# Optimization experiments

Hardware: AMD Instinct MI355X
Metric: run time of the kernel (lower is better)

Reference implementation:

```python
import jax, jax.numpy as jnp
import numpy as np

N_NODES = 100000
N_EDGES = 1600000
N_GRAPHS = 64
D_IN = 3
HIDDEN = 256
N_CLASSES = 10
NEG_SLOPE = 0.01  # torch F.leaky_relu default


def gcn_conv(x, W, b, src, dst, n_nodes):
    """GCNConv: D^{-1/2}(A+I)D^{-1/2} X W + b with self-loops."""
    h = x @ W  # [N, H]
    ones = jnp.ones(src.shape[0], h.dtype)
    deg = jax.ops.segment_sum(ones, dst, num_segments=n_nodes) + 1.0  # +1 self-loop
    dinv = jax.lax.rsqrt(deg)
    coef = dinv[src] * dinv[dst]  # [E]
    agg = jax.ops.segment_sum(h[src] * coef[:, None], dst, num_segments=n_nodes)
    agg = agg + h * (1.0 / deg)[:, None]  # self-loop contribution (norm = 1/deg)
    return agg + b


def leaky_relu(v):
    return jnp.where(v >= 0, v, NEG_SLOPE * v)


def setup_inputs() -> dict:
    key = jax.random.key(0)
    ks = jax.random.split(key, 12)
    x = jax.random.normal(ks[0], (N_NODES, D_IN), dtype=jnp.float32)
    edge_index = jax.random.randint(ks[1], (2, N_EDGES), 0, N_NODES, dtype=jnp.int32)
    batch = jnp.sort(jax.random.randint(ks[2], (N_NODES,), 0, N_GRAPHS, dtype=jnp.int32))
    s1 = 1.0 / np.sqrt(D_IN)
    s2 = 1.0 / np.sqrt(HIDDEN)
    W1 = jax.random.uniform(ks[3], (D_IN, HIDDEN), jnp.float32, -s1, s1)
    b1 = jnp.zeros((HIDDEN,), jnp.float32)
    W2 = jax.random.uniform(ks[4], (HIDDEN, HIDDEN), jnp.float32, -s2, s2)
    b2 = jnp.zeros((HIDDEN,), jnp.float32)
    W3 = jax.random.uniform(ks[5], (HIDDEN, HIDDEN), jnp.float32, -s2, s2)
    b3 = jnp.zeros((HIDDEN,), jnp.float32)
    Wc = jax.random.uniform(ks[6], (HIDDEN, N_CLASSES), jnp.float32, -s2, s2)
    bc = jax.random.uniform(ks[7], (N_CLASSES,), jnp.float32, -s2, s2)
    return {"x": x, "edge_index": edge_index, "batch": batch,
            "W1": W1, "b1": b1, "W2": W2, "b2": b2, "W3": W3, "b3": b3,
            "Wc": Wc, "bc": bc}


def reference(x, edge_index, batch, W1, b1, W2, b2, W3, b3, Wc, bc):
    src, dst = edge_index[0], edge_index[1]
    h = leaky_relu(gcn_conv(x, W1, b1, src, dst, N_NODES))
    h = leaky_relu(gcn_conv(h, W2, b2, src, dst, N_NODES))
    h = leaky_relu(gcn_conv(h, W3, b3, src, dst, N_NODES))
    # global mean pool over graphs
    sums = jax.ops.segment_sum(h, batch, num_segments=N_GRAPHS)
    cnt = jax.ops.segment_sum(jnp.ones((N_NODES,), h.dtype), batch, num_segments=N_GRAPHS)
    pooled = sums / jnp.maximum(cnt, 1.0)[:, None]  # [G, H]
    logits = pooled @ Wc + bc
    return jax.nn.softmax(logits, axis=1)
```

## Files before the change

### kernel.cpp

```cpp
#include <hip/hip_runtime.h>
#include <hip/hip_bf16.h>
#include <cstdint>
#include <cstddef>

#define N_NODES   100000
#define N_EDGES   1600000
#define N_GRAPHS  64
#define HIDDEN    256
#define N_CLASSES 10
#define NEG_SLOPE 0.01f

#define E_PAD    (N_EDGES + 8 * N_NODES)
#define N_RANGES 8
#define R_SIZE   ((N_NODES + N_RANGES - 1) / N_RANGES)
#define CHUNK    2048
#define GEMM_BLOCKS 391

typedef __attribute__((ext_vector_type(4))) float f32x4;
typedef __attribute__((ext_vector_type(2))) float f32x2;

__device__ __forceinline__ float bf2f(unsigned short u) {
    return __uint_as_float(((unsigned int)u) << 16);
}

__device__ __forceinline__ unsigned char f2fp8(float v) {
    return (unsigned char)(__builtin_amdgcn_cvt_pk_fp8_f32(v, v, 0, false) & 0xff);
}

__global__ void k_deg_hist(const int* __restrict__ dst, int* __restrict__ cnt) {
    int e = (blockIdx.x * 256 + threadIdx.x) * 4;
    if (e >= N_EDGES) return;
    int4 d4 = *(const int4*)(dst + e);
    atomicAdd(&cnt[d4.x], 1);
    atomicAdd(&cnt[d4.y], 1);
    atomicAdd(&cnt[d4.z], 1);
    atomicAdd(&cnt[d4.w], 1);
}

__global__ void k_graph_bounds(const int* __restrict__ batch,
                               int* __restrict__ gstart, int* __restrict__ gcnt) {
    int g = threadIdx.x;
    int lo = 0, hi = N_NODES;
    while (lo < hi) { int mid = (lo + hi) >> 1; if (batch[mid] < g) lo = mid + 1; else hi = mid; }
    __shared__ int sh[N_GRAPHS + 1];
    sh[g] = lo;
    if (g == 0) sh[N_GRAPHS] = N_NODES;
    __syncthreads();
    gstart[g] = sh[g];
    gcnt[g]   = sh[g + 1] - sh[g];
}

__global__ void k_dinv(const int* __restrict__ cnt, float* __restrict__ dinv) {
    int i = blockIdx.x * 256 + threadIdx.x;
    if (i < N_NODES) dinv[i] = rsqrtf((float)cnt[i] + 1.0f);
}

__global__ void k_scanA(const int* __restrict__ cnt, int* __restrict__ out, int* __restrict__ bsum) {
    __shared__ int sh[256];
    int tid = threadIdx.x;
    int base = blockIdx.x * 1024 + tid * 4;
    int v[4]; int s = 0;
#pragma unroll
    for (int i = 0; i < 4; i++) {
        int idx = base + i;
        v[i] = (idx < N_NODES) ? ((cnt[idx] + 7) & ~7) : 0;
        s += v[i];
    }
    sh[tid] = s; __syncthreads();
    for (int off = 1; off < 256; off <<= 1) {
        int t = (tid >= off) ? sh[tid - off] : 0;
        __syncthreads();
        sh[tid] += t;
        __syncthreads();
    }
    int excl = sh[tid] - s;
    if (tid == 255) bsum[blockIdx.x] = sh[255];
#pragma unroll
    for (int i = 0; i < 4; i++) { int idx = base + i; if (idx < N_NODES) out[idx] = excl; excl += v[i]; }
}

__global__ void k_scanB(int* __restrict__ bsum, int nb) {
    __shared__ int sh[128];
    int tid = threadIdx.x;
    int v = (tid < nb) ? bsum[tid] : 0;
    sh[tid] = v; __syncthreads();
    for (int off = 1; off < 128; off <<= 1) {
        int t = (tid >= off) ? sh[tid - off] : 0;
        __syncthreads();
        sh[tid] += t;
        __syncthreads();
    }
    if (tid < nb) bsum[tid] = sh[tid] - v;
}

__global__ void k_scanC(int* __restrict__ off_arr, const int* __restrict__ bsum,
                        int* __restrict__ cursor, const int* __restrict__ cnt,
                        int2* __restrict__ rec) {
    int i = blockIdx.x * 256 + threadIdx.x;
    if (i < N_NODES) {
        int v = off_arr[i] + bsum[i >> 10];
        off_arr[i] = v;
        cursor[i]  = v;
        int c  = cnt[i];
        int cp = (c + 7) & ~7;
        for (int p = v + c; p < v + cp; ++p) rec[p] = make_int2(0, 0);
        if (i == N_NODES - 1) off_arr[N_NODES] = v + cp;
    }
}

__global__ __launch_bounds__(256) void k_fill(const int* __restrict__ src, const int* __restrict__ dst,
                                              const float* __restrict__ dinv,
                                              int* __restrict__ cursor, int2* __restrict__ rec) {
    int b = blockIdx.x;
    int r = b & (N_RANGES - 1);
    int lo = r * R_SIZE, hi = lo + R_SIZE;
    int e0 = (b >> 3) * CHUNK + threadIdx.x * 8;
    if (e0 >= N_EDGES) return;
    if (e0 + 8 <= N_EDGES) {
        int4 da = *(const int4*)(dst + e0);
        int4 db = *(const int4*)(dst + e0 + 4);
        int d[8] = {da.x, da.y, da.z, da.w, db.x, db.y, db.z, db.w};
#pragma unroll
        for (int j = 0; j < 8; ++j) {
            if (d[j] >= lo && d[j] < hi) {
                int s = src[e0 + j];
                float c = dinv[s] * dinv[d[j]];
                int p = atomicAdd(&cursor[d[j]], 1);
                rec[p] = make_int2(s, __float_as_int(c));
            }
        }
    } else {
        for (int j = 0; j < 8 && e0 + j < N_EDGES; ++j) {
            int dj = dst[e0 + j];
            if (dj >= lo && dj < hi) {
                int s = src[e0 + j];
                float c = dinv[s] * dinv[dj];
                int p = atomicAdd(&cursor[dj], 1);
                rec[p] = make_int2(s, __float_as_int(c));
            }
        }
    }
}

__global__ void k_wprep(const float* __restrict__ W, unsigned char* __restrict__ Wswz) {
    int n = blockIdx.x; int k = threadIdx.x;
    unsigned char v = f2fp8(W[k * HIDDEN + n]);
    int k0 = k >> 5, nt = n >> 4;
    int lane = (((k >> 3) & 3) << 4) | (n & 15);
    int j = k & 7;
    Wswz[(size_t)(((k0 * 16) + nt) * 64 + lane) * 8 + j] = v;
}

__global__ void k_agg3(const float* __restrict__ x, const int* __restrict__ off,
                       const int2* __restrict__ rec, const float* __restrict__ dinv,
                       float4* __restrict__ ax) {
    int i = blockIdx.x * 256 + threadIdx.x;
    if (i >= N_NODES) return;
    float di = dinv[i];
    float selfc = di * di;
    float a0 = x[i * 3 + 0] * selfc, a1 = x[i * 3 + 1] * selfc, a2 = x[i * 3 + 2] * selfc;
    int e = off[i], e1 = off[i + 1];
    for (; e < e1; e += 4) {
        const int4* rp = (const int4*)(rec + e);
        int4 r01 = rp[0];
        int4 r23 = rp[1];
        int s0 = r01.x, s1 = r01.z, s2 = r23.x, s3 = r23.z;
        float c0 = __int_as_float(r01.y), c1 = __int_as_float(r01.w);
        float c2 = __int_as_float(r23.y), c3 = __int_as_float(r23.w);
        a0 += c0 * x[s0 * 3 + 0] + c1 * x[s1 * 3 + 0] + c2 * x[s2 * 3 + 0] + c3 * x[s3 * 3 + 0];
        a1 += c0 * x[s0 * 3 + 1] + c1 * x[s1 * 3 + 1] + c2 * x[s2 * 3 + 1] + c3 * x[s3 * 3 + 1];
        a2 += c0 * x[s0 * 3 + 2] + c1 * x[s1 * 3 + 2] + c2 * x[s2 * 3 + 2] + c3 * x[s3 * 3 + 2];
    }
    ax[i] = make_float4(a0, a1, a2, 0.f);
}

__global__ void k_l1(const float4* __restrict__ ax, const float* __restrict__ W1,
                     const float* __restrict__ b1, unsigned char* __restrict__ out) {
    int node = blockIdx.x; int c = threadIdx.x;
    float4 a = ax[node];
    float v = a.x * W1[c] + a.y * W1[HIDDEN + c] + a.z * W1[2 * HIDDEN + c] + b1[c];
    v = v >= 0.f ? v : NEG_SLOPE * v;
    out[(size_t)node * HIDDEN + c] = f2fp8(v);
}

__global__ __launch_bounds__(512, 2) void k_gemm_mfma(const unsigned char* __restrict__ A,
                                                      const unsigned char* __restrict__ Wswz,
                                                      unsigned char* __restrict__ C, int M) {
    __shared__ long Bs[8192];
    int tid = threadIdx.x;
    {
        const float4* gsrc = (const float4*)Wswz;
        float4* ldst = (float4*)Bs;
#pragma unroll
        for (int i = 0; i < 8; ++i) ldst[tid + 512 * i] = gsrc[tid + 512 * i];
    }
    __syncthreads();
    int lane = tid & 63, wv = tid >> 6;
    int quad = lane >> 4, r = lane & 15;
    int nstrips = M >> 4;
    for (int s = blockIdx.x * 8 + wv; s < nstrips; s += gridDim.x * 8) {
        int m0 = s * 16;
        const long* Ab = (const long*)(A + (size_t)(m0 + r) * HIDDEN) + quad;
        long af[8];
#pragma unroll
        for (int k0 = 0; k0 < 8; ++k0) af[k0] = Ab[k0 * 4];
#pragma unroll
        for (int half = 0; half < 2; ++half) {
            f32x4 acc[8];
#pragma unroll
            for (int i = 0; i < 8; i++) acc[i] = (f32x4){0.f, 0.f, 0.f, 0.f};
#pragma unroll
            for (int k0 = 0; k0 < 8; ++k0) {
#pragma unroll
                for (int nt = 0; nt < 8; ++nt) {
                    long b = Bs[(k0 * 16 + half * 8 + nt) * 64 + lane];
                    acc[nt] = __builtin_amdgcn_mfma_f32_16x16x32_fp8_fp8(af[k0], b, acc[nt], 0, 0, 0);
                }
            }
#pragma unroll
            for (int nt = 0; nt < 8; ++nt) {
#pragma unroll
                for (int i = 0; i < 4; ++i) {
                    int row = m0 + quad * 4 + i;
                    C[(size_t)row * HIDDEN + (half * 8 + nt) * 16 + r] = f2fp8(acc[nt][i]);
                }
            }
        }
    }
}

__global__ __launch_bounds__(256) void k_agg(const unsigned char* __restrict__ h,
                                             const float* __restrict__ bias,
                                             const int* __restrict__ off, const int2* __restrict__ rec,
                                             const float* __restrict__ dinv,
                                             unsigned char* __restrict__ out) {
    int node = (blockIdx.x * 256 + threadIdx.x) >> 6;
    int lane = threadIdx.x & 63;
    if (node >= N_NODES) return;
    float di = dinv[node];
    float selfc = di * di;
    unsigned int hv = *(const unsigned int*)(h + (size_t)node * HIDDEN + lane * 4);
    f32x2 hlo = __builtin_amdgcn_cvt_pk_f32_fp8(hv, false);
    f32x2 hhi = __builtin_amdgcn_cvt_pk_f32_fp8(hv, true);
    float4 bv = ((const float4*)bias)[lane];
    float4 acc = make_float4(bv.x + hlo.x * selfc, bv.y + hlo.y * selfc,
                             bv.z + hhi.x * selfc, bv.w + hhi.y * selfc);
    int e = off[node], e1 = off[node + 1];
    for (; e < e1; e += 8) {
        const int4* rp = (const int4*)(rec + e);
        int4 ra = rp[0];
        int4 rb = rp[1];
        int4 rc = rp[2];
        int4 rd = rp[3];
        unsigned int w0 = *(const unsigned int*)(h + (size_t)ra.x * HIDDEN + lane * 4);
        unsigned int w1 = *(const unsigned int*)(h + (size_t)ra.z * HIDDEN + lane * 4);
        unsigned int w2 = *(const unsigned int*)(h + (size_t)rb.x * HIDDEN + lane * 4);
        unsigned int w3 = *(const unsigned int*)(h + (size_t)rb.z * HIDDEN + lane * 4);
        unsigned int w4 = *(const unsigned int*)(h + (size_t)rc.x * HIDDEN + lane * 4);
        unsigned int w5 = *(const unsigned int*)(h + (size_t)rc.z * HIDDEN + lane * 4);
        unsigned int w6 = *(const unsigned int*)(h + (size_t)rd.x * HIDDEN + lane * 4);
        unsigned int w7 = *(const unsigned int*)(h + (size_t)rd.z * HIDDEN + lane * 4);
        float c0 = __int_as_float(ra.y), c1 = __int_as_float(ra.w);
        float c2 = __int_as_float(rb.y), c3 = __int_as_float(rb.w);
        float c4 = __int_as_float(rc.y), c5 = __int_as_float(rc.w);
        float c6 = __int_as_float(rd.y), c7 = __int_as_float(rd.w);
        f32x2 l0 = __builtin_amdgcn_cvt_pk_f32_fp8(w0, false), g0 = __builtin_amdgcn_cvt_pk_f32_fp8(w0, true);
        f32x2 l1 = __builtin_amdgcn_cvt_pk_f32_fp8(w1, false), g1 = __builtin_amdgcn_cvt_pk_f32_fp8(w1, true);
        f32x2 l2 = __builtin_amdgcn_cvt_pk_f32_fp8(w2, false), g2 = __builtin_amdgcn_cvt_pk_f32_fp8(w2, true);
        f32x2 l3 = __builtin_amdgcn_cvt_pk_f32_fp8(w3, false), g3 = __builtin_amdgcn_cvt_pk_f32_fp8(w3, true);
        f32x2 l4 = __builtin_amdgcn_cvt_pk_f32_fp8(w4, false), g4 = __builtin_amdgcn_cvt_pk_f32_fp8(w4, true);
        f32x2 l5 = __builtin_amdgcn_cvt_pk_f32_fp8(w5, false), g5 = __builtin_amdgcn_cvt_pk_f32_fp8(w5, true);
        f32x2 l6 = __builtin_amdgcn_cvt_pk_f32_fp8(w6, false), g6 = __builtin_amdgcn_cvt_pk_f32_fp8(w6, true);
        f32x2 l7 = __builtin_amdgcn_cvt_pk_f32_fp8(w7, false), g7 = __builtin_amdgcn_cvt_pk_f32_fp8(w7, true);
        acc.x += c0 * l0.x + c1 * l1.x + c2 * l2.x + c3 * l3.x
               + c4 * l4.x + c5 * l5.x + c6 * l6.x + c7 * l7.x;
        acc.y += c0 * l0.y + c1 * l1.y + c2 * l2.y + c3 * l3.y
               + c4 * l4.y + c5 * l5.y + c6 * l6.y + c7 * l7.y;
        acc.z += c0 * g0.x + c1 * g1.x + c2 * g2.x + c3 * g3.x
               + c4 * g4.x + c5 * g5.x + c6 * g6.x + c7 * g7.x;
        acc.w += c0 * g0.y + c1 * g1.y + c2 * g2.y + c3 * g3.y
               + c4 * g4.y + c5 * g5.y + c6 * g6.y + c7 * g7.y;
    }
    acc.x = acc.x >= 0.f ? acc.x : NEG_SLOPE * acc.x;
    acc.y = acc.y >= 0.f ? acc.y : NEG_SLOPE * acc.y;
    acc.z = acc.z >= 0.f ? acc.z : NEG_SLOPE * acc.z;
    acc.w = acc.w >= 0.f ? acc.w : NEG_SLOPE * acc.w;
    unsigned int pk = __builtin_amdgcn_cvt_pk_fp8_f32(acc.x, acc.y, 0, false);
    pk = __builtin_amdgcn_cvt_pk_fp8_f32(acc.z, acc.w, pk, true);
    *(unsigned int*)(out + (size_t)node * HIDDEN + lane * 4) = pk;
}

__global__ void k_pool(const unsigned char* __restrict__ h, const int* __restrict__ gstart,
                       const int* __restrict__ gcnt, float* __restrict__ pooled) {
    int g = blockIdx.x, chunk = blockIdx.y, t = threadIdx.x;
    int s = gstart[g], c = gcnt[g];
    int i0 = s + (int)(((long long)c * chunk) / 16);
    int i1 = s + (int)(((long long)c * (chunk + 1)) / 16);
    float acc = 0.f;
    for (int i = i0; i < i1; ++i) {
        f32x2 v = __builtin_amdgcn_cvt_pk_f32_fp8((unsigned int)h[(size_t)i * HIDDEN + t], false);
        acc += v.x;
    }
    atomicAdd(&pooled[g * HIDDEN + t], acc);
}

__global__ void k_head(const float* __restrict__ pooled, const int* __restrict__ gcnt,
                       const float* __restrict__ Wc, const float* __restrict__ bc,
                       float* __restrict__ out) {
    int g = blockIdx.x; int l = threadIdx.x;
    float inv = 1.0f / fmaxf((float)gcnt[g], 1.0f);
    float p[4];
#pragma unroll
    for (int i = 0; i < 4; i++) p[i] = pooled[g * HIDDEN + l + i * 64] * inv;
    __shared__ float logits[N_CLASSES];
#pragma unroll
    for (int j = 0; j < N_CLASSES; j++) {
        float s = 0.f;
#pragma unroll
        for (int i = 0; i < 4; i++) s += p[i] * Wc[(l + i * 64) * N_CLASSES + j];
        for (int o = 32; o > 0; o >>= 1) s += __shfl_down(s, o, 64);
        if (l == 0) logits[j] = s + bc[j];
    }
    __syncthreads();
    if (l == 0) {
        float m = logits[0];
        for (int j = 1; j < N_CLASSES; j++) m = fmaxf(m, logits[j]);
        float e[N_CLASSES]; float sum = 0.f;
        for (int j = 0; j < N_CLASSES; j++) { e[j] = expf(logits[j] - m); sum += e[j]; }
        for (int j = 0; j < N_CLASSES; j++) out[g * N_CLASSES + j] = e[j] / sum;
    }
}

extern "C" void kernel_launch(void* const* d_in, const int* in_sizes, int n_in,
                              void* d_out, int out_size, void* d_ws, size_t ws_size,
                              hipStream_t stream) {
    const float* x     = (const float*)d_in[0];
    const int*   edge  = (const int*)d_in[1];
    const int*   batch = (const int*)d_in[2];
    const float* W1 = (const float*)d_in[3];
    const float* b1 = (const float*)d_in[4];
    const float* W2 = (const float*)d_in[5];
    const float* b2 = (const float*)d_in[6];
    const float* W3 = (const float*)d_in[7];
    const float* b3 = (const float*)d_in[8];
    const float* Wc = (const float*)d_in[9];
    const float* bc = (const float*)d_in[10];
    float* out = (float*)d_out;
    const int* srcp = edge;
    const int* dstp = edge + N_EDGES;

    char* ws = (char*)d_ws;
    size_t off = 0;
    auto alloc = [&](size_t bytes) -> char* {
        char* p = ws + off;
        off += (bytes + 255) & ~(size_t)255;
        return p;
    };
    unsigned char* hA   = (unsigned char*)alloc((size_t)N_NODES * HIDDEN);
    unsigned char* hB   = (unsigned char*)alloc((size_t)N_NODES * HIDDEN);
    unsigned char* Wz2  = (unsigned char*)alloc((size_t)HIDDEN * HIDDEN);
    unsigned char* Wz3  = (unsigned char*)alloc((size_t)HIDDEN * HIDDEN);
    int*   deg_cnt  = (int*)alloc((size_t)N_NODES * 4);
    float* dinv     = (float*)alloc((size_t)N_NODES * 4);
    int*   csr_off  = (int*)alloc((size_t)(N_NODES + 1) * 4);
    int*   cursor   = (int*)alloc((size_t)N_NODES * 4);
    int2*  csr_rec  = (int2*)alloc((size_t)E_PAD * 8);
    float4* ax      = (float4*)alloc((size_t)N_NODES * 16);
    int*   gcnt     = (int*)alloc((size_t)N_GRAPHS * 4);
    int*   gstart   = (int*)alloc((size_t)N_GRAPHS * 4);
    float* pooled   = (float*)alloc((size_t)N_GRAPHS * HIDDEN * 4);
    int*   bsum     = (int*)alloc(128 * 4);

    hipMemsetAsync(deg_cnt, 0, (size_t)N_NODES * 4, stream);
    hipMemsetAsync(pooled, 0, (size_t)N_GRAPHS * HIDDEN * 4, stream);

    int eb4 = (N_EDGES / 4 + 255) / 256;
    int nb  = (N_NODES + 255) / 256;
    int sblocks = (N_NODES + 1023) / 1024;
    int fillb = N_RANGES * ((N_EDGES + CHUNK - 1) / CHUNK);

    k_deg_hist<<<eb4, 256, 0, stream>>>(dstp, deg_cnt);
    k_graph_bounds<<<1, 64, 0, stream>>>(batch, gstart, gcnt);
    k_dinv<<<nb, 256, 0, stream>>>(deg_cnt, dinv);
    k_scanA<<<sblocks, 256, 0, stream>>>(deg_cnt, csr_off, bsum);
    k_scanB<<<1, 128, 0, stream>>>(bsum, sblocks);
    k_scanC<<<nb, 256, 0, stream>>>(csr_off, bsum, cursor, deg_cnt, csr_rec);
    k_fill<<<fillb, 256, 0, stream>>>(srcp, dstp, dinv, cursor, csr_rec);
    k_wprep<<<HIDDEN, HIDDEN, 0, stream>>>(W2, Wz2);
    k_wprep<<<HIDDEN, HIDDEN, 0, stream>>>(W3, Wz3);

    k_agg3<<<nb, 256, 0, stream>>>(x, csr_off, csr_rec, dinv, ax);
    k_l1<<<N_NODES, 256, 0, stream>>>(ax, W1, b1, hA);

    int aggb = (N_NODES + 3) / 4;
    k_gemm_mfma<<<GEMM_BLOCKS, 512, 0, stream>>>(hA, Wz2, hB, N_NODES);
    k_agg<<<aggb, 256, 0, stream>>>(hB, b2, csr_off, csr_rec, dinv, hA);
    k_gemm_mfma<<<GEMM_BLOCKS, 512, 0, stream>>>(hA, Wz3, hB, N_NODES);
    k_agg<<<aggb, 256, 0, stream>>>(hB, b3, csr_off, csr_rec, dinv, hA);
    dim3 pg(N_GRAPHS, 16);
    k_pool<<<pg, 256, 0, stream>>>(hA, gstart, gcnt, pooled);
    k_head<<<N_GRAPHS, 64, 0, stream>>>(pooled, gcnt, Wc, bc, out);
}
```

Baseline: 550.4 us.

## Range-partition degree histogram, add nontemporal edge loads, pad x to float4

The degree histogram now uses the same dst-range partitioned blocks as the fill kernel, so each block's atomics land in one eighth of the node array. Edge and CSR record reads in fill and both aggregation kernels become nontemporal vector loads, keeping streamed data from pushing gathered features out of cache. The input features are padded to float4 by a new kernel so layer-1 aggregation gathers one vector per neighbour instead of three scalars. The tail-guard branch in fill is removed, which relies on N_EDGES being a multiple of 8. The histogram now reads dst eight times, and the extra launch and buffer add cost.

```diff
diff --git a/kernel.cpp b/kernel.cpp
--- a/kernel.cpp
+++ b/kernel.cpp
@@ -18,6 +18,7 @@
 
 typedef __attribute__((ext_vector_type(4))) float f32x4;
 typedef __attribute__((ext_vector_type(2))) float f32x2;
+typedef __attribute__((ext_vector_type(4))) int   v4i;
 
 __device__ __forceinline__ float bf2f(unsigned short u) {
     return __uint_as_float(((unsigned int)u) << 16);
@@ -27,14 +28,19 @@
     return (unsigned char)(__builtin_amdgcn_cvt_pk_fp8_f32(v, v, 0, false) & 0xff);
 }
 
-__global__ void k_deg_hist(const int* __restrict__ dst, int* __restrict__ cnt) {
-    int e = (blockIdx.x * 256 + threadIdx.x) * 4;
-    if (e >= N_EDGES) return;
-    int4 d4 = *(const int4*)(dst + e);
-    atomicAdd(&cnt[d4.x], 1);
-    atomicAdd(&cnt[d4.y], 1);
-    atomicAdd(&cnt[d4.z], 1);
-    atomicAdd(&cnt[d4.w], 1);
+__global__ __launch_bounds__(256) void k_deg_hist(const int* __restrict__ dst, int* __restrict__ cnt) {
+    int b = blockIdx.x;
+    int r = b & (N_RANGES - 1);
+    int lo = r * R_SIZE, hi = lo + R_SIZE;
+    int e0 = (b >> 3) * CHUNK + threadIdx.x * 8;
+    if (e0 >= N_EDGES) return;
+    v4i da = __builtin_nontemporal_load((const v4i*)(dst + e0));
+    v4i db = __builtin_nontemporal_load((const v4i*)(dst + e0 + 4));
+    int d[8] = {da.x, da.y, da.z, da.w, db.x, db.y, db.z, db.w};
+#pragma unroll
+    for (int j = 0; j < 8; ++j) {
+        if (d[j] >= lo && d[j] < hi) atomicAdd(&cnt[d[j]], 1);
+    }
 }
 
 __global__ void k_graph_bounds(const int* __restrict__ batch,
@@ -53,6 +59,11 @@
 __global__ void k_dinv(const int* __restrict__ cnt, float* __restrict__ dinv) {
     int i = blockIdx.x * 256 + threadIdx.x;
     if (i < N_NODES) dinv[i] = rsqrtf((float)cnt[i] + 1.0f);
+}
+
+__global__ void k_xpad(const float* __restrict__ x, float4* __restrict__ xp) {
+    int i = blockIdx.x * 256 + threadIdx.x;
+    if (i < N_NODES) xp[i] = make_float4(x[i * 3 + 0], x[i * 3 + 1], x[i * 3 + 2], 0.f);
 }
 
 __global__ void k_scanA(const int* __restrict__ cnt, int* __restrict__ out, int* __restrict__ bsum) {
@@ -116,28 +127,18 @@
     int lo = r * R_SIZE, hi = lo + R_SIZE;
     int e0 = (b >> 3) * CHUNK + threadIdx.x * 8;
     if (e0 >= N_EDGES) return;
-    if (e0 + 8 <= N_EDGES) {
-        int4 da = *(const int4*)(dst + e0);
-        int4 db = *(const int4*)(dst + e0 + 4);
-        int d[8] = {da.x, da.y, da.z, da.w, db.x, db.y, db.z, db.w};
-#pragma unroll
-        for (int j = 0; j < 8; ++j) {
-            if (d[j] >= lo && d[j] < hi) {
-                int s = src[e0 + j];
-                float c = dinv[s] * dinv[d[j]];
-                int p = atomicAdd(&cursor[d[j]], 1);
-                rec[p] = make_int2(s, __float_as_int(c));
-            }
-        }
-    } else {
-        for (int j = 0; j < 8 && e0 + j < N_EDGES; ++j) {
-            int dj = dst[e0 + j];
-            if (dj >= lo && dj < hi) {
-                int s = src[e0 + j];
-                float c = dinv[s] * dinv[dj];
-                int p = atomicAdd(&cursor[dj], 1);
-                rec[p] = make_int2(s, __float_as_int(c));
-            }
+    v4i da = __builtin_nontemporal_load((const v4i*)(dst + e0));
+    v4i db = __builtin_nontemporal_load((const v4i*)(dst + e0 + 4));
+    v4i sa = __builtin_nontemporal_load((const v4i*)(src + e0));
+    v4i sb = __builtin_nontemporal_load((const v4i*)(src + e0 + 4));
+    int d[8] = {da.x, da.y, da.z, da.w, db.x, db.y, db.z, db.w};
+    int s[8] = {sa.x, sa.y, sa.z, sa.w, sb.x, sb.y, sb.z, sb.w};
+#pragma unroll
+    for (int j = 0; j < 8; ++j) {
+        if (d[j] >= lo && d[j] < hi) {
+            float c = dinv[s[j]] * dinv[d[j]];
+            int p = atomicAdd(&cursor[d[j]], 1);
+            rec[p] = make_int2(s[j], __float_as_int(c));
         }
     }
 }
@@ -151,25 +152,26 @@
     Wswz[(size_t)(((k0 * 16) + nt) * 64 + lane) * 8 + j] = v;
 }
 
-__global__ void k_agg3(const float* __restrict__ x, const int* __restrict__ off,
+__global__ void k_agg3(const float4* __restrict__ xp, const int* __restrict__ off,
                        const int2* __restrict__ rec, const float* __restrict__ dinv,
                        float4* __restrict__ ax) {
     int i = blockIdx.x * 256 + threadIdx.x;
     if (i >= N_NODES) return;
     float di = dinv[i];
     float selfc = di * di;
-    float a0 = x[i * 3 + 0] * selfc, a1 = x[i * 3 + 1] * selfc, a2 = x[i * 3 + 2] * selfc;
+    float4 xi = xp[i];
+    float a0 = xi.x * selfc, a1 = xi.y * selfc, a2 = xi.z * selfc;
     int e = off[i], e1 = off[i + 1];
     for (; e < e1; e += 4) {
-        const int4* rp = (const int4*)(rec + e);
-        int4 r01 = rp[0];
-        int4 r23 = rp[1];
-        int s0 = r01.x, s1 = r01.z, s2 = r23.x, s3 = r23.z;
+        const v4i* rp = (const v4i*)(rec + e);
+        v4i r01 = __builtin_nontemporal_load(rp);
+        v4i r23 = __builtin_nontemporal_load(rp + 1);
+        float4 x0 = xp[r01.x], x1 = xp[r01.z], x2 = xp[r23.x], x3 = xp[r23.z];
         float c0 = __int_as_float(r01.y), c1 = __int_as_float(r01.w);
         float c2 = __int_as_float(r23.y), c3 = __int_as_float(r23.w);
-        a0 += c0 * x[s0 * 3 + 0] + c1 * x[s1 * 3 + 0] + c2 * x[s2 * 3 + 0] + c3 * x[s3 * 3 + 0];
-        a1 += c0 * x[s0 * 3 + 1] + c1 * x[s1 * 3 + 1] + c2 * x[s2 * 3 + 1] + c3 * x[s3 * 3 + 1];
-        a2 += c0 * x[s0 * 3 + 2] + c1 * x[s1 * 3 + 2] + c2 * x[s2 * 3 + 2] + c3 * x[s3 * 3 + 2];
+        a0 += c0 * x0.x + c1 * x1.x + c2 * x2.x + c3 * x3.x;
+        a1 += c0 * x0.y + c1 * x1.y + c2 * x2.y + c3 * x3.y;
+        a2 += c0 * x0.z + c1 * x1.z + c2 * x2.z + c3 * x3.z;
     }
     ax[i] = make_float4(a0, a1, a2, 0.f);
 }
@@ -247,11 +249,11 @@
                              bv.z + hhi.x * selfc, bv.w + hhi.y * selfc);
     int e = off[node], e1 = off[node + 1];
     for (; e < e1; e += 8) {
-        const int4* rp = (const int4*)(rec + e);
-        int4 ra = rp[0];
-        int4 rb = rp[1];
-        int4 rc = rp[2];
-        int4 rd = rp[3];
+        const v4i* rp = (const v4i*)(rec + e);
+        v4i ra = __builtin_nontemporal_load(rp);
+        v4i rb = __builtin_nontemporal_load(rp + 1);
+        v4i rc = __builtin_nontemporal_load(rp + 2);
+        v4i rd = __builtin_nontemporal_load(rp + 3);
         unsigned int w0 = *(const unsigned int*)(h + (size_t)ra.x * HIDDEN + lane * 4);
         unsigned int w1 = *(const unsigned int*)(h + (size_t)ra.z * HIDDEN + lane * 4);
         unsigned int w2 = *(const unsigned int*)(h + (size_t)rb.x * HIDDEN + lane * 4);
@@ -366,6 +368,7 @@
     int*   cursor   = (int*)alloc((size_t)N_NODES * 4);
     int2*  csr_rec  = (int2*)alloc((size_t)E_PAD * 8);
     float4* ax      = (float4*)alloc((size_t)N_NODES * 16);
+    float4* xp      = (float4*)alloc((size_t)N_NODES * 16);
     int*   gcnt     = (int*)alloc((size_t)N_GRAPHS * 4);
     int*   gstart   = (int*)alloc((size_t)N_GRAPHS * 4);
     float* pooled   = (float*)alloc((size_t)N_GRAPHS * HIDDEN * 4);
@@ -374,14 +377,14 @@
     hipMemsetAsync(deg_cnt, 0, (size_t)N_NODES * 4, stream);
     hipMemsetAsync(pooled, 0, (size_t)N_GRAPHS * HIDDEN * 4, stream);
 
-    int eb4 = (N_EDGES / 4 + 255) / 256;
     int nb  = (N_NODES + 255) / 256;
     int sblocks = (N_NODES + 1023) / 1024;
     int fillb = N_RANGES * ((N_EDGES + CHUNK - 1) / CHUNK);
 
-    k_deg_hist<<<eb4, 256, 0, stream>>>(dstp, deg_cnt);
+    k_deg_hist<<<fillb, 256, 0, stream>>>(dstp, deg_cnt);
     k_graph_bounds<<<1, 64, 0, stream>>>(batch, gstart, gcnt);
     k_dinv<<<nb, 256, 0, stream>>>(deg_cnt, dinv);
+    k_xpad<<<nb, 256, 0, stream>>>(x, xp);
     k_scanA<<<sblocks, 256, 0, stream>>>(deg_cnt, csr_off, bsum);
     k_scanB<<<1, 128, 0, stream>>>(bsum, sblocks);
     k_scanC<<<nb, 256, 0, stream>>>(csr_off, bsum, cursor, deg_cnt, csr_rec);
@@ -389,7 +392,7 @@
     k_wprep<<<HIDDEN, HIDDEN, 0, stream>>>(W2, Wz2);
     k_wprep<<<HIDDEN, HIDDEN, 0, stream>>>(W3, Wz3);
 
-    k_agg3<<<nb, 256, 0, stream>>>(x, csr_off, csr_rec, dinv, ax);
+    k_agg3<<<nb, 256, 0, stream>>>(xp, csr_off, csr_rec, dinv, ax);
     k_l1<<<N_NODES, 256, 0, stream>>>(ax, W1, b1, hA);
 
     int aggb = (N_NODES + 3) / 4;
```

New measurement: 586.6 us. 1.07x slower.
